# Kernel optimization log

Hardware: AMD Instinct MI355X
Metric: run time of the kernel (lower is better)

## Reference

```python
import jax, jax.numpy as jnp
import numpy as np

N_NODES = 50000
N_EDGES = 800000
IN_C, OUT_C, EDGE_F, HEADS, HID, FINAL = 8, 16, 8, 4, 64, 128
NEG_SLOPE = 0.2  # PyG GATConv default LeakyReLU slope


def setup_inputs() -> dict:
    key = jax.random.key(0)
    ks = jax.random.split(key, 12)
    s = 0.1
    return {
        "x": jax.random.normal(ks[0], (N_NODES, IN_C), jnp.float32),
        "edge_index": jax.random.randint(ks[1], (2, N_EDGES), 0, N_NODES, jnp.int64),
        "edge_attr": jax.random.normal(ks[2], (N_EDGES, EDGE_F), jnp.float32),
        # NNConv params: root weight, bias, edge-MLP Linear(EDGE_F -> IN_C*OUT_C)
        "ecc_root": jax.random.normal(ks[3], (IN_C, OUT_C), jnp.float32) * s,
        "ecc_bias": jnp.zeros((OUT_C,), jnp.float32),
        "mlp_w": jax.random.normal(ks[4], (EDGE_F, IN_C * OUT_C), jnp.float32) * s,
        "mlp_b": jnp.zeros((IN_C * OUT_C,), jnp.float32),
        # GATConv params
        "gat_lin": jax.random.normal(ks[5], (OUT_C, HEADS * HID), jnp.float32) * s,
        "att_src": jax.random.normal(ks[6], (HEADS, HID), jnp.float32) * s,
        "att_dst": jax.random.normal(ks[7], (HEADS, HID), jnp.float32) * s,
        "gat_bias": jnp.zeros((HEADS * HID,), jnp.float32),
        # final Linear
        "fc_w": jax.random.normal(ks[8], (HEADS * HID, FINAL), jnp.float32) * s,
        "fc_b": jnp.zeros((FINAL,), jnp.float32),
    }


def _forward(x, edge_index, edge_attr, ecc_root, ecc_bias, mlp_w, mlp_b,
             gat_lin, att_src, att_dst, gat_bias, fc_w, fc_b):
    src, dst = edge_index[0], edge_index[1]  # messages flow src -> dst

    # ---- NNConv (edge-conditioned conv), aggr='add' ----
    # per-edge weight matrices [E, IN_C, OUT_C] from edge MLP
    w_e = (edge_attr @ mlp_w + mlp_b).reshape(-1, IN_C, OUT_C)
    msg = jnp.einsum('ei,eio->eo', x[src], w_e)                 # [E, OUT_C]
    agg = jax.ops.segment_sum(msg, dst, num_segments=N_NODES)   # [N, OUT_C]
    h = jax.nn.relu(x @ ecc_root + agg + ecc_bias)              # [N, OUT_C]

    # ---- GATConv (heads concatenated) ----
    g = (h @ gat_lin).reshape(N_NODES, HEADS, HID)              # [N, H, D]
    a_src = jnp.einsum('nhd,hd->nh', g, att_src)                # [N, H]
    a_dst = jnp.einsum('nhd,hd->nh', g, att_dst)
    e = jax.nn.leaky_relu(a_src[src] + a_dst[dst], NEG_SLOPE)   # [E, H]
    # segment softmax over incoming edges of each dst node
    e_max = jax.ops.segment_max(e, dst, num_segments=N_NODES)   # [N, H]
    e_max = jnp.where(jnp.isfinite(e_max), e_max, 0.0)
    e_exp = jnp.exp(e - e_max[dst])                             # [E, H]
    denom = jax.ops.segment_sum(e_exp, dst, num_segments=N_NODES)
    alpha = e_exp / (denom[dst] + 1e-16)                        # [E, H]
    out = jax.ops.segment_sum(alpha[:, :, None] * g[src], dst,
                              num_segments=N_NODES)             # [N, H, D]
    out = jax.nn.relu(out.reshape(N_NODES, HEADS * HID) + gat_bias)

    # ---- final linear ----
    return out @ fc_w + fc_b                                    # [N, FINAL]


def reference(x, edge_index, edge_attr, ecc_root, ecc_bias, mlp_w, mlp_b,
              gat_lin, att_src, att_dst, gat_bias, fc_w, fc_b):
    return _forward(x, edge_index, edge_attr, ecc_root, ecc_bias, mlp_w, mlp_b,
                    gat_lin, att_src, att_dst, gat_bias, fc_w, fc_b)
```

## Files before the change

### kernel.cpp

```cpp
#include <hip/hip_runtime.h>

#define N_NODES 50000
#define N_EDGES 800000
#define IN_C 8
#define OUT_C 16
#define EDGE_F 8
#define HEADS 4
#define HID 64
#define GDIM (HEADS*HID)
#define FINAL 128
#define NEG_SLOPE 0.2f
#define EB ((N_EDGES+255)/256)
#define NBLK 196

__device__ __forceinline__ int clampn(int v) {
    return v < 0 ? 0 : (v >= N_NODES ? N_NODES - 1 : v);
}

__global__ __launch_bounds__(256) void k_histfold(
    const int* __restrict__ dst, int* __restrict__ cnt, int* __restrict__ rnk,
    const float* __restrict__ gat_lin,
    const float* __restrict__ att_src_w, const float* __restrict__ att_dst_w,
    float* __restrict__ wsrc, float* __restrict__ wdst)
{
    if (blockIdx.x < EB) {
        int e = blockIdx.x * 256 + threadIdx.x;
        if (e >= N_EDGES) return;
        rnk[e] = atomicAdd(&cnt[clampn(dst[e])], 1);
    } else {
        int t = threadIdx.x;
        if (t >= 64) return;
        int c = t >> 2, h = t & 3;
        float ws = 0.f, wd = 0.f;
        for (int k = 0; k < HID; k++) {
            float l = gat_lin[c * GDIM + h * HID + k];
            ws += l * att_src_w[h * HID + k];
            wd += l * att_dst_w[h * HID + k];
        }
        wsrc[t] = ws;
        wdst[t] = wd;
    }
}

__global__ __launch_bounds__(256) void k_part(const int* __restrict__ cnt,
                                              int* __restrict__ part)
{
    int i = blockIdx.x * 256 + threadIdx.x;
    int v = (i < N_NODES) ? cnt[i] : 0;
#pragma unroll
    for (int off = 32; off; off >>= 1) v += __shfl_down(v, off);
    __shared__ int ws[4];
    if ((threadIdx.x & 63) == 0) ws[threadIdx.x >> 6] = v;
    __syncthreads();
    if (threadIdx.x == 0) part[blockIdx.x] = ws[0] + ws[1] + ws[2] + ws[3];
}

__global__ __launch_bounds__(256) void k_scan1(const int* __restrict__ part,
                                               int* __restrict__ partscan)
{
    int t = threadIdx.x;
    int v = (t < NBLK) ? part[t] : 0;
    int lane = t & 63, wid = t >> 6;
    int incl = v;
#pragma unroll
    for (int off = 1; off < 64; off <<= 1) {
        int u = __shfl_up(incl, off);
        if (lane >= off) incl += u;
    }
    __shared__ int wsum[4];
    if (lane == 63) wsum[wid] = incl;
    __syncthreads();
    int add = 0;
    for (int w = 0; w < wid; w++) add += wsum[w];
    partscan[t] = incl - v + add;
}

__global__ __launch_bounds__(256) void k_add(const int* __restrict__ cnt,
                                             const int* __restrict__ partscan,
                                             int* __restrict__ offs)
{
    int i = blockIdx.x * 256 + threadIdx.x;
    int v = (i < N_NODES) ? cnt[i] : 0;
    int lane = threadIdx.x & 63, wid = threadIdx.x >> 6;
    int incl = v;
#pragma unroll
    for (int off = 1; off < 64; off <<= 1) {
        int u = __shfl_up(incl, off);
        if (lane >= off) incl += u;
    }
    __shared__ int wsum[4];
    if (lane == 63) wsum[wid] = incl;
    __syncthreads();
    int add = partscan[blockIdx.x];
    for (int w = 0; w < wid; w++) add += wsum[w];
    if (i < N_NODES) offs[i] = incl - v + add;
    if (i == 0) offs[N_NODES] = N_EDGES;
}

__global__ __launch_bounds__(256) void k_scatter(
    const int* __restrict__ src, const int* __restrict__ dst,
    const int* __restrict__ rnk, const int* __restrict__ offs,
    int2* __restrict__ se_csr)
{
    int e = blockIdx.x * 256 + threadIdx.x;
    if (e >= N_EDGES) return;
    int p = offs[clampn(dst[e])] + rnk[e];
    se_csr[p] = make_int2(clampn(src[e]), e);
}

__global__ __launch_bounds__(256) void k2T_wave(
    const float* __restrict__ x,
    const int2* __restrict__ se_csr, const int* __restrict__ offs,
    const float* __restrict__ ea,
    const float* __restrict__ mlp_w, const float* __restrict__ mlp_b,
    const float* __restrict__ ecc_root, const float* __restrict__ ecc_bias,
    const float* __restrict__ wsrc, const float* __restrict__ wdst,
    float* __restrict__ h_tab, float* __restrict__ asrc, float* __restrict__ adst)
{
    __shared__ float smW[64 * 17];
    __shared__ float smb[128];
    __shared__ float sroot[128];
    __shared__ float sbias[16];
    __shared__ float sws[64], swd[64];
    __shared__ float sT[4][64];
    __shared__ float sxs[4][8];

    int t = threadIdx.x;
    for (int idx = t; idx < 1024; idx += 256)
        smW[(idx >> 4) * 17 + (idx & 15)] = mlp_w[idx];
    if (t < 128) smb[t] = mlp_b[t];
    if (t >= 128 && t < 256) sroot[t - 128] = ecc_root[t - 128];
    if (t < 16) sbias[t] = ecc_bias[t];
    if (t >= 32 && t < 96) sws[t - 32] = wsrc[t - 32];
    if (t >= 96 && t < 160) swd[t - 96] = wdst[t - 96];

    int wid = t >> 6, lane = t & 63;
    int n = blockIdx.x * 4 + wid;
    int f = lane >> 3, i = lane & 7;
    int beg = offs[n], end = offs[n + 1];

    float t0 = 0.f, t1 = 0.f, t2 = 0.f, t3 = 0.f, xs = 0.f;
    int j = beg;
    if (j + 3 < end) {
        int2 se0 = se_csr[j],     se1 = se_csr[j + 1];
        int2 se2 = se_csr[j + 2], se3 = se_csr[j + 3];
        float a0 = ea[(unsigned)se0.y * EDGE_F + f];
        float a1 = ea[(unsigned)se1.y * EDGE_F + f];
        float a2 = ea[(unsigned)se2.y * EDGE_F + f];
        float a3 = ea[(unsigned)se3.y * EDGE_F + f];
        float x0 = x[(unsigned)se0.x * IN_C + i];
        float x1 = x[(unsigned)se1.x * IN_C + i];
        float x2 = x[(unsigned)se2.x * IN_C + i];
        float x3 = x[(unsigned)se3.x * IN_C + i];
        j += 4;
        for (; j + 3 < end; j += 4) {
            int2 ne0 = se_csr[j],     ne1 = se_csr[j + 1];
            int2 ne2 = se_csr[j + 2], ne3 = se_csr[j + 3];
            float na0 = ea[(unsigned)ne0.y * EDGE_F + f];
            float na1 = ea[(unsigned)ne1.y * EDGE_F + f];
            float na2 = ea[(unsigned)ne2.y * EDGE_F + f];
            float na3 = ea[(unsigned)ne3.y * EDGE_F + f];
            float nx0 = x[(unsigned)ne0.x * IN_C + i];
            float nx1 = x[(unsigned)ne1.x * IN_C + i];
            float nx2 = x[(unsigned)ne2.x * IN_C + i];
            float nx3 = x[(unsigned)ne3.x * IN_C + i];
            t0 += a0 * x0; t1 += a1 * x1; t2 += a2 * x2; t3 += a3 * x3;
            xs += (x0 + x1) + (x2 + x3);
            a0 = na0; a1 = na1; a2 = na2; a3 = na3;
            x0 = nx0; x1 = nx1; x2 = nx2; x3 = nx3;
        }
        t0 += a0 * x0; t1 += a1 * x1; t2 += a2 * x2; t3 += a3 * x3;
        xs += (x0 + x1) + (x2 + x3);
    }
    for (; j < end; j++) {
        int2 se = se_csr[j];
        float a = ea[(unsigned)se.y * EDGE_F + f];
        float xv = x[(unsigned)se.x * IN_C + i];
        t0 += a * xv;
        xs += xv;
    }
    sT[wid][lane] = (t0 + t1) + (t2 + t3);
    if (f == 0) sxs[wid][i] = xs;
    __syncthreads();

    int o = lane & 15, p = lane >> 4;
    float v = 0.f;
#pragma unroll
    for (int q2 = 0; q2 < 16; q2++) {
        int jj = p * 16 + q2;
        v += smW[jj * 17 + o] * sT[wid][jj];
    }
    v += __shfl_down(v, 32);
    v += __shfl_down(v, 16);

    float hv = 0.f;
    if (lane < 16) {
        float vv = v + sbias[o];
#pragma unroll
        for (int ii = 0; ii < IN_C; ii++) {
            vv += smb[ii * 16 + o] * sxs[wid][ii];
            vv += x[n * IN_C + ii] * sroot[ii * 16 + o];
        }
        hv = fmaxf(vv, 0.f);
        h_tab[n * OUT_C + o] = hv;
    }
    float as = 0.f, ad = 0.f;
    int h2 = lane & 3;
#pragma unroll
    for (int c = 0; c < 16; c++) {
        float hc = __shfl(hv, c);
        as += hc * sws[c * 4 + h2];
        ad += hc * swd[c * 4 + h2];
    }
    if (lane < 4) {
        asrc[n * HEADS + lane] = as;
        adst[n * HEADS + lane] = ad;
    }
}

__global__ __launch_bounds__(256) void k_gatE(
    const int* __restrict__ offs, const int2* __restrict__ se_csr,
    const float* __restrict__ asrc, const float* __restrict__ adst,
    const float* __restrict__ h_tab, float* __restrict__ U_all)
{
    int t = threadIdx.x;
    int wid = t >> 6, lane = t & 63;
    int n = blockIdx.x * 4 + wid;
    int h = lane >> 4, c = lane & 15;
    float adsth = adst[n * HEADS + h];
    int beg = offs[n], end = offs[n + 1];

    float U = 0.f, den = 0.f;
    int j = beg;
    if (j + 3 < end) {
        int s0 = se_csr[j].x,     s1 = se_csr[j + 1].x;
        int s2 = se_csr[j + 2].x, s3 = se_csr[j + 3].x;
        float av0 = asrc[(unsigned)s0 * HEADS + h], av1 = asrc[(unsigned)s1 * HEADS + h];
        float av2 = asrc[(unsigned)s2 * HEADS + h], av3 = asrc[(unsigned)s3 * HEADS + h];
        float h0 = h_tab[(unsigned)s0 * OUT_C + c], h1 = h_tab[(unsigned)s1 * OUT_C + c];
        float h2v = h_tab[(unsigned)s2 * OUT_C + c], h3v = h_tab[(unsigned)s3 * OUT_C + c];
        j += 4;
        for (; j + 3 < end; j += 4) {
            int ns0 = se_csr[j].x,     ns1 = se_csr[j + 1].x;
            int ns2 = se_csr[j + 2].x, ns3 = se_csr[j + 3].x;
            float nav0 = asrc[(unsigned)ns0 * HEADS + h];
            float nav1 = asrc[(unsigned)ns1 * HEADS + h];
            float nav2 = asrc[(unsigned)ns2 * HEADS + h];
            float nav3 = asrc[(unsigned)ns3 * HEADS + h];
            float nh0 = h_tab[(unsigned)ns0 * OUT_C + c];
            float nh1 = h_tab[(unsigned)ns1 * OUT_C + c];
            float nh2 = h_tab[(unsigned)ns2 * OUT_C + c];
            float nh3 = h_tab[(unsigned)ns3 * OUT_C + c];
            float v0 = av0 + adsth; v0 = v0 > 0.f ? v0 : NEG_SLOPE * v0;
            float v1 = av1 + adsth; v1 = v1 > 0.f ? v1 : NEG_SLOPE * v1;
            float v2 = av2 + adsth; v2 = v2 > 0.f ? v2 : NEG_SLOPE * v2;
            float v3 = av3 + adsth; v3 = v3 > 0.f ? v3 : NEG_SLOPE * v3;
            float p0 = __expf(v0), p1 = __expf(v1), p2 = __expf(v2), p3 = __expf(v3);
            den += (p0 + p1) + (p2 + p3);
            U += p0 * h0 + p1 * h1 + p2 * h2v + p3 * h3v;
            av0 = nav0; av1 = nav1; av2 = nav2; av3 = nav3;
            h0 = nh0; h1 = nh1; h2v = nh2; h3v = nh3;
        }
        float v0 = av0 + adsth; v0 = v0 > 0.f ? v0 : NEG_SLOPE * v0;
        float v1 = av1 + adsth; v1 = v1 > 0.f ? v1 : NEG_SLOPE * v1;
        float v2 = av2 + adsth; v2 = v2 > 0.f ? v2 : NEG_SLOPE * v2;
        float v3 = av3 + adsth; v3 = v3 > 0.f ? v3 : NEG_SLOPE * v3;
        float p0 = __expf(v0), p1 = __expf(v1), p2 = __expf(v2), p3 = __expf(v3);
        den += (p0 + p1) + (p2 + p3);
        U += p0 * h0 + p1 * h1 + p2 * h2v + p3 * h3v;
    }
    for (; j < end; j++) {
        int s = se_csr[j].x;
        float av = asrc[(unsigned)s * HEADS + h];
        float hvv = h_tab[(unsigned)s * OUT_C + c];
        float v = av + adsth; v = v > 0.f ? v : NEG_SLOPE * v;
        float pe = __expf(v);
        den += pe;
        U += pe * hvv;
    }
    U_all[(size_t)n * 64 + lane] = U / (den + 1e-16f);
}

#define FBM 64
__global__ __launch_bounds__(256) void k_fuse(
    const float* __restrict__ U_all, const float* __restrict__ gat_lin,
    const float* __restrict__ gat_bias, const float* __restrict__ fc_w,
    const float* __restrict__ fc_b, float* __restrict__ y)
{
    __shared__ float slin[16 * GDIM];
    __shared__ float sA[16][FBM + 4];
    __shared__ float sW[16][FINAL];
    int tid = threadIdx.x;
    int r0 = blockIdx.x * FBM;

    for (int idx = tid; idx < (16 * GDIM) / 4; idx += 256)
        ((float4*)slin)[idx] = ((const float4*)gat_lin)[idx];
    __syncthreads();

    int ar  = tid >> 2;
    int akq = (tid & 3) * 4;
    int grow = r0 + ar;

    int rg = tid >> 4;
    int cg = tid & 15;

    int skk = tid >> 4;
    int scc = (tid & 15) * 4;

    float acc[4][8];
#pragma unroll
    for (int r = 0; r < 4; r++)
#pragma unroll
        for (int c = 0; c < 8; c++) acc[r][c] = 0.f;

    for (int h = 0; h < HEADS; ++h) {
        float4 ua = make_float4(0.f, 0.f, 0.f, 0.f), ub = ua, uc4 = ua, ud = ua;
        if (grow < N_NODES) {
            const float4* up = (const float4*)&U_all[(size_t)grow * 64 + h * 16];
            ua = up[0]; ub = up[1]; uc4 = up[2]; ud = up[3];
        }
        float ureg[16] = {ua.x, ua.y, ua.z, ua.w,  ub.x, ub.y, ub.z, ub.w,
                          uc4.x, uc4.y, uc4.z, uc4.w,  ud.x, ud.y, ud.z, ud.w};

#pragma unroll
        for (int tt = 0; tt < 4; ++tt) {
            int k0 = h * 64 + tt * 16;
            float4 bv = *(const float4*)&gat_bias[k0 + akq];
            float g0 = 0.f, g1 = 0.f, g2 = 0.f, g3 = 0.f;
#pragma unroll
            for (int c = 0; c < 16; ++c) {
                float4 lv = *(const float4*)&slin[c * GDIM + k0 + akq];
                g0 += ureg[c] * lv.x;
                g1 += ureg[c] * lv.y;
                g2 += ureg[c] * lv.z;
                g3 += ureg[c] * lv.w;
            }
            __syncthreads();
            sA[akq + 0][ar] = fmaxf(g0 + bv.x, 0.f);
            sA[akq + 1][ar] = fmaxf(g1 + bv.y, 0.f);
            sA[akq + 2][ar] = fmaxf(g2 + bv.z, 0.f);
            sA[akq + 3][ar] = fmaxf(g3 + bv.w, 0.f);
            {
                const float* wrow = &fc_w[(size_t)(k0 + skk) * FINAL];
                *(float4*)&sW[skk][scc]      = *(const float4*)&wrow[scc];
                *(float4*)&sW[skk][scc + 64] = *(const float4*)&wrow[scc + 64];
            }
            __syncthreads();
#pragma unroll
            for (int kk = 0; kk < 16; ++kk) {
                float4 a  = *(const float4*)&sA[kk][rg * 4];
                float4 w0 = *(const float4*)&sW[kk][cg * 4];
                float4 w1 = *(const float4*)&sW[kk][cg * 4 + 64];
                float av[4] = {a.x, a.y, a.z, a.w};
#pragma unroll
                for (int r = 0; r < 4; r++) {
                    acc[r][0] += av[r] * w0.x;
                    acc[r][1] += av[r] * w0.y;
                    acc[r][2] += av[r] * w0.z;
                    acc[r][3] += av[r] * w0.w;
                    acc[r][4] += av[r] * w1.x;
                    acc[r][5] += av[r] * w1.y;
                    acc[r][6] += av[r] * w1.z;
                    acc[r][7] += av[r] * w1.w;
                }
            }
        }
    }

    float4 fb0 = *(const float4*)&fc_b[cg * 4];
    float4 fb1 = *(const float4*)&fc_b[cg * 4 + 64];
#pragma unroll
    for (int r = 0; r < 4; r++) {
        int row = r0 + rg * 4 + r;
        if (row < N_NODES) {
            float* yp = &y[(size_t)row * FINAL];
            *(float4*)&yp[cg * 4] =
                make_float4(acc[r][0] + fb0.x, acc[r][1] + fb0.y,
                            acc[r][2] + fb0.z, acc[r][3] + fb0.w);
            *(float4*)&yp[cg * 4 + 64] =
                make_float4(acc[r][4] + fb1.x, acc[r][5] + fb1.y,
                            acc[r][6] + fb1.z, acc[r][7] + fb1.w);
        }
    }
}

extern "C" void kernel_launch(void* const* d_in, const int* in_sizes, int n_in,
                              void* d_out, int out_size, void* d_ws, size_t ws_size,
                              hipStream_t stream)
{
    const float* x        = (const float*)d_in[0];
    const int*   ei       = (const int*)d_in[1];
    const float* ea       = (const float*)d_in[2];
    const float* ecc_root = (const float*)d_in[3];
    const float* ecc_bias = (const float*)d_in[4];
    const float* mlp_w    = (const float*)d_in[5];
    const float* mlp_b    = (const float*)d_in[6];
    const float* gat_lin  = (const float*)d_in[7];
    const float* att_src  = (const float*)d_in[8];
    const float* att_dst  = (const float*)d_in[9];
    const float* gat_bias = (const float*)d_in[10];
    const float* fc_w     = (const float*)d_in[11];
    const float* fc_b     = (const float*)d_in[12];
    float* y = (float*)d_out;

    const int* src = ei;
    const int* dst = ei + N_EDGES;

    float* h_tab = (float*)d_ws;
    float* U_all = h_tab + (size_t)N_NODES * OUT_C;
    float* asrc  = U_all + (size_t)N_NODES * 64;
    float* adst  = asrc + (size_t)N_NODES * HEADS;
    float* wsrc  = adst + (size_t)N_NODES * HEADS;
    float* wdst  = wsrc + 64;
    int*   cnt      = (int*)(wdst + 64);
    int*   offs     = cnt + N_NODES;
    int*   part     = offs + N_NODES + 1;
    int*   partscan = part + 256;
    int*   rnk      = partscan + 256;
    int2*  se_csr   = (int2*)(rnk + N_EDGES + 1);

    hipMemsetAsync(cnt, 0, sizeof(int) * N_NODES, stream);

    k_histfold<<<EB + 1, 256, 0, stream>>>(dst, cnt, rnk, gat_lin, att_src, att_dst,
                                           wsrc, wdst);
    k_part    <<<NBLK, 256, 0, stream>>>(cnt, part);
    k_scan1   <<<1, 256, 0, stream>>>(part, partscan);
    k_add     <<<NBLK, 256, 0, stream>>>(cnt, partscan, offs);
    k_scatter <<<EB, 256, 0, stream>>>(src, dst, rnk, offs, se_csr);

    k2T_wave  <<<N_NODES / 4, 256, 0, stream>>>(x, se_csr, offs, ea, mlp_w, mlp_b,
                                                ecc_root, ecc_bias, wsrc, wdst,
                                                h_tab, asrc, adst);
    k_gatE    <<<N_NODES / 4, 256, 0, stream>>>(offs, se_csr, asrc, adst, h_tab, U_all);
    k_fuse    <<<(N_NODES + FBM - 1) / FBM, 256, 0, stream>>>(U_all, gat_lin, gat_bias,
                                                              fc_w, fc_b, y);
}
```

Before: 310.4 us.

## Split final fused GEMM output columns across two blocks per row tile

The final fused kernel now assigns each block a 64-row by 64-column output tile instead of 64 by 128, and doubles the grid. This increases the block count and halves the accumulator registers per thread, which should improve occupancy and load balance. In exchange, each row tile's GAT projection and bias/ReLU work is recomputed by both column blocks, and the U_all reads are doubled.

Measured after the change: 318.6 us. 2.6% more time.

```diff
diff --git a/kernel.cpp b/kernel.cpp
--- a/kernel.cpp
+++ b/kernel.cpp
@@ -282,6 +282,7 @@
 }
 
 #define FBM 64
+#define FBN 64
 __global__ __launch_bounds__(256) void k_fuse(
     const float* __restrict__ U_all, const float* __restrict__ gat_lin,
     const float* __restrict__ gat_bias, const float* __restrict__ fc_w,
@@ -289,9 +290,10 @@
 {
     __shared__ float slin[16 * GDIM];
     __shared__ float sA[16][FBM + 4];
-    __shared__ float sW[16][FINAL];
+    __shared__ float sW[16][FBN];
     int tid = threadIdx.x;
-    int r0 = blockIdx.x * FBM;
+    int r0 = (blockIdx.x >> 1) * FBM;
+    int c0 = (blockIdx.x & 1) * FBN;
 
     for (int idx = tid; idx < (16 * GDIM) / 4; idx += 256)
         ((float4*)slin)[idx] = ((const float4*)gat_lin)[idx];
@@ -307,11 +309,11 @@
     int skk = tid >> 4;
     int scc = (tid & 15) * 4;
 
-    float acc[4][8];
+    float acc[4][4];
 #pragma unroll
     for (int r = 0; r < 4; r++)
 #pragma unroll
-        for (int c = 0; c < 8; c++) acc[r][c] = 0.f;
+        for (int c = 0; c < 4; c++) acc[r][c] = 0.f;
 
     for (int h = 0; h < HEADS; ++h) {
         float4 ua = make_float4(0.f, 0.f, 0.f, 0.f), ub = ua, uc4 = ua, ud = ua;
@@ -340,46 +342,33 @@
             sA[akq + 1][ar] = fmaxf(g1 + bv.y, 0.f);
             sA[akq + 2][ar] = fmaxf(g2 + bv.z, 0.f);
             sA[akq + 3][ar] = fmaxf(g3 + bv.w, 0.f);
-            {
-                const float* wrow = &fc_w[(size_t)(k0 + skk) * FINAL];
-                *(float4*)&sW[skk][scc]      = *(const float4*)&wrow[scc];
-                *(float4*)&sW[skk][scc + 64] = *(const float4*)&wrow[scc + 64];
-            }
+            *(float4*)&sW[skk][scc] =
+                *(const float4*)&fc_w[(size_t)(k0 + skk) * FINAL + c0 + scc];
             __syncthreads();
 #pragma unroll
             for (int kk = 0; kk < 16; ++kk) {
-                float4 a  = *(const float4*)&sA[kk][rg * 4];
-                float4 w0 = *(const float4*)&sW[kk][cg * 4];
-                float4 w1 = *(const float4*)&sW[kk][cg * 4 + 64];
+                float4 a = *(const float4*)&sA[kk][rg * 4];
+                float4 w = *(const float4*)&sW[kk][cg * 4];
                 float av[4] = {a.x, a.y, a.z, a.w};
 #pragma unroll
                 for (int r = 0; r < 4; r++) {
-                    acc[r][0] += av[r] * w0.x;
-                    acc[r][1] += av[r] * w0.y;
-                    acc[r][2] += av[r] * w0.z;
-                    acc[r][3] += av[r] * w0.w;
-                    acc[r][4] += av[r] * w1.x;
-                    acc[r][5] += av[r] * w1.y;
-                    acc[r][6] += av[r] * w1.z;
-                    acc[r][7] += av[r] * w1.w;
+                    acc[r][0] += av[r] * w.x;
+                    acc[r][1] += av[r] * w.y;
+                    acc[r][2] += av[r] * w.z;
+                    acc[r][3] += av[r] * w.w;
                 }
             }
         }
     }
 
-    float4 fb0 = *(const float4*)&fc_b[cg * 4];
-    float4 fb1 = *(const float4*)&fc_b[cg * 4 + 64];
+    float4 fb = *(const float4*)&fc_b[c0 + cg * 4];
 #pragma unroll
     for (int r = 0; r < 4; r++) {
         int row = r0 + rg * 4 + r;
         if (row < N_NODES) {
-            float* yp = &y[(size_t)row * FINAL];
-            *(float4*)&yp[cg * 4] =
-                make_float4(acc[r][0] + fb0.x, acc[r][1] + fb0.y,
-                            acc[r][2] + fb0.z, acc[r][3] + fb0.w);
-            *(float4*)&yp[cg * 4 + 64] =
-                make_float4(acc[r][4] + fb1.x, acc[r][5] + fb1.y,
-                            acc[r][6] + fb1.z, acc[r][7] + fb1.w);
+            *(float4*)&y[(size_t)row * FINAL + c0 + cg * 4] =
+                make_float4(acc[r][0] + fb.x, acc[r][1] + fb.y,
+                            acc[r][2] + fb.z, acc[r][3] + fb.w);
         }
     }
 }
@@ -432,6 +421,7 @@
                                                 ecc_root, ecc_bias, wsrc, wdst,
                                                 h_tab, asrc, adst);
     k_gatE    <<<N_NODES / 4, 256, 0, stream>>>(offs, se_csr, asrc, adst, h_tab, U_all);
-    k_fuse    <<<(N_NODES + FBM - 1) / FBM, 256, 0, stream>>>(U_all, gat_lin, gat_bias,
-                                                              fc_w, fc_b, y);
-}
+    k_fuse    <<<((N_NODES + FBM - 1) / FBM) * 2, 256, 0, stream>>>(U_all, gat_lin,
+                                                                    gat_bias, fc_w,
+                                                                    fc_b, y);
+}
```
